# Optimization experiments

Hardware: AMD Instinct MI355X
Metric: run time of the kernel (lower is better)

The kernel has to match this reference:

```python
import jax, jax.numpy as jnp
import numpy as np

B, S, D = 4, 2048, 1024
H, HD = 16, 64
DFF = 4096
EPS = 1e-6


def setup_inputs() -> dict:
    key = jax.random.key(0)
    ks = jax.random.split(key, 16)
    sc = 0.02
    def w(k, shape):
        return jax.random.normal(k, shape, dtype=jnp.float32) * sc
    return {
        'x': jax.random.normal(ks[0], (B, S, D), dtype=jnp.float32),
        'wq': w(ks[1], (D, D)), 'bq': jnp.zeros((D,), jnp.float32),
        'wk': w(ks[2], (D, D)), 'bk': jnp.zeros((D,), jnp.float32),
        'wv': w(ks[3], (D, D)), 'bv': jnp.zeros((D,), jnp.float32),
        'wo': w(ks[4], (D, D)), 'bo': jnp.zeros((D,), jnp.float32),
        'w1': w(ks[5], (D, DFF)), 'b1': jnp.zeros((DFF,), jnp.float32),
        'w2': w(ks[6], (DFF, D)), 'b2': jnp.zeros((D,), jnp.float32),
        'ln1_a': jnp.ones((D,), jnp.float32), 'ln1_b': jnp.zeros((D,), jnp.float32),
        'ln2_a': jnp.ones((D,), jnp.float32), 'ln2_b': jnp.zeros((D,), jnp.float32),
    }


def layernorm(x, alpha, bias):
    # Matches torch module: std is unbiased (ddof=1), divide by (std + eps)
    mean = jnp.mean(x, axis=-1, keepdims=True)
    var = jnp.sum((x - mean) ** 2, axis=-1, keepdims=True) / (x.shape[-1] - 1)
    std = jnp.sqrt(var)
    return alpha * ((x - mean) / (std + EPS)) + bias


def mha(x, wq, bq, wk, bk, wv, bv, wo, bo):
    q = (x @ wq + bq).reshape(B, S, H, HD)
    k = (x @ wk + bk).reshape(B, S, H, HD)
    v = (x @ wv + bv).reshape(B, S, H, HD)
    scores = jnp.einsum('bqhd,bkhd->bhqk', q, k) / jnp.sqrt(jnp.float32(HD))
    attn = jax.nn.softmax(scores, axis=-1)
    out = jnp.einsum('bhqk,bkhd->bqhd', attn, v).reshape(B, S, D)
    return out @ wo + bo


def reference(x, wq, bq, wk, bk, wv, bv, wo, bo, w1, b1, w2, b2,
              ln1_a, ln1_b, ln2_a, ln2_b):
    # Residual 1: x + MHA(LN(x))   (dropout = identity, eval mode)
    x = x + mha(layernorm(x, ln1_a, ln1_b), wq, bq, wk, bk, wv, bv, wo, bo)
    # Residual 2: x + FFN(LN(x))
    h = layernorm(x, ln2_a, ln2_b)
    ffn = jax.nn.relu(h @ w1 + b1) @ w2 + b2
    return x + ffn
```

## Files before the change

### kernel.cpp

```cpp
#include <hip/hip_runtime.h>

#define S_ 2048
#define D_ 1024

typedef unsigned short u16;
typedef unsigned int u32;
typedef __bf16 bf16x8 __attribute__((ext_vector_type(8)));
typedef unsigned short us8 __attribute__((ext_vector_type(8)));
typedef unsigned short us4 __attribute__((ext_vector_type(4)));
typedef unsigned int u32x4 __attribute__((ext_vector_type(4)));
typedef float f32x4 __attribute__((ext_vector_type(4)));

#if __has_builtin(__builtin_amdgcn_exp2f)
#define EXP2(x) __builtin_amdgcn_exp2f(x)
#else
#define EXP2(x) exp2f(x)
#endif

static __device__ __forceinline__ u16 f2bf(float f) {
  unsigned u = __builtin_bit_cast(unsigned, f);
  u += 0x7fffu + ((u >> 16) & 1u);
  return (u16)(u >> 16);
}

static __device__ __forceinline__ unsigned cvtpk_bf16(float lo, float hi) {
  unsigned r;
  asm("v_cvt_pk_bf16_f32 %0, %1, %2" : "=v"(r) : "v"(lo), "v"(hi));
  return r;
}

static __device__ __forceinline__ f32x4 mfma16(bf16x8 a, bf16x8 b, f32x4 c) {
  return __builtin_amdgcn_mfma_f32_16x16x32_bf16(a, b, c, 0, 0, 0);
}

static __device__ __forceinline__ void gload16(const void* g, void* lds) {
  __builtin_amdgcn_global_load_lds((const __attribute__((address_space(1))) void*)g,
                                   (__attribute__((address_space(3))) void*)lds, 16, 0, 0);
}

__global__ __launch_bounds__(256) void prep_kernel(
    const float* __restrict__ wq, const float* __restrict__ wk, const float* __restrict__ wv,
    const float* __restrict__ wo, const float* __restrict__ w1, const float* __restrict__ w2,
    const float* __restrict__ bq, const float* __restrict__ bk, const float* __restrict__ bv,
    u16* __restrict__ wqkv, u16* __restrict__ wot, u16* __restrict__ w1t,
    u16* __restrict__ w2t, float* __restrict__ bcat, float qs) {
  const int bid = blockIdx.x;
  const int tx = threadIdx.x, ty = threadIdx.y;
  if (bid >= 12288) {
    const int i = (bid - 12288) * 256 + ty * 32 + tx;
    bcat[i] = (i < 1024) ? bq[i] * qs : ((i < 2048) ? bk[i - 1024] : bv[i - 2048]);
    return;
  }
  const float* in;
  u16* out;
  int K, N, idx;
  float sc = 1.0f;
  if (bid < 4096) {
    K = 1024; N = 1024; idx = bid & 1023;
    if (bid < 1024)      { in = wq; out = wqkv;             sc = qs; }
    else if (bid < 2048) { in = wk; out = wqkv + (1 << 20); }
    else if (bid < 3072) { in = wv; out = wqkv + (2 << 20); }
    else                 { in = wo; out = wot; }
  } else if (bid < 8192) {
    in = w1; out = w1t; K = 1024; N = 4096; idx = bid - 4096;
  } else {
    in = w2; out = w2t; K = 4096; N = 1024; idx = bid - 8192;
  }
  const int nb = N >> 5;
  const int n0 = (idx % nb) * 32, k0 = (idx / nb) * 32;
  __shared__ float t[32][33];
#pragma unroll
  for (int i = 0; i < 4; i++)
    t[ty + 8 * i][tx] = in[(size_t)(k0 + ty + 8 * i) * N + n0 + tx];
  __syncthreads();
#pragma unroll
  for (int i = 0; i < 4; i++)
    out[(size_t)(n0 + ty + 8 * i) * K + k0 + tx] = f2bf(t[tx][ty + 8 * i] * sc);
}

__global__ __launch_bounds__(256) void ln_kernel(const float* __restrict__ in,
                                                 u16* __restrict__ out,
                                                 const float* __restrict__ alpha,
                                                 const float* __restrict__ beta) {
  const int row = blockIdx.x;
  const int tid = threadIdx.x;
  const float4 v = *(const float4*)(in + (size_t)row * D_ + tid * 4);
  float s = v.x + v.y + v.z + v.w;
  float ss = v.x * v.x + v.y * v.y + v.z * v.z + v.w * v.w;
#pragma unroll
  for (int off = 32; off >= 1; off >>= 1) {
    s += __shfl_xor(s, off);
    ss += __shfl_xor(ss, off);
  }
  __shared__ float red[8];
  const int w = tid >> 6, lane = tid & 63;
  if (lane == 0) { red[w] = s; red[4 + w] = ss; }
  __syncthreads();
  s = red[0] + red[1] + red[2] + red[3];
  ss = red[4] + red[5] + red[6] + red[7];
  const float mean = s * (1.0f / D_);
  const float var = (ss - s * mean) * (1.0f / (D_ - 1));
  const float inv = 1.0f / (sqrtf(var) + 1e-6f);
  const int j = tid * 4;
  const float4 av = *(const float4*)(alpha + j);
  const float4 bv = *(const float4*)(beta + j);
  us4 o;
  o[0] = f2bf((v.x - mean) * inv * av.x + bv.x);
  o[1] = f2bf((v.y - mean) * inv * av.y + bv.y);
  o[2] = f2bf((v.z - mean) * inv * av.z + bv.z);
  o[3] = f2bf((v.w - mean) * inv * av.w + bv.w);
  *(us4*)(out + (size_t)row * D_ + j) = o;
}

template <int OM, bool RELU, bool RESID>
__global__ __launch_bounds__(512, 2) void gemm_bt(const u16* __restrict__ A,
                                                  const u16* __restrict__ Bt,
                                                  const float* __restrict__ bias,
                                                  const float* __restrict__ resid,
                                                  void* __restrict__ outp,
                                                  void* __restrict__ out1,
                                                  void* __restrict__ out2, int N, int K) {
  __shared__ u16 lds[3 * 24576];
  const int tid = threadIdx.x;
  const int lane = tid & 63, w = tid >> 6;
  const int g = lane >> 4, r = lane & 15;
  const int wr = w >> 1, wc = w & 1;

  const int gx = gridDim.x;
  const int nwg = gx * gridDim.y;
  const int orig = blockIdx.y * gx + blockIdx.x;
  const int nid = (orig & 7) * (nwg >> 3) + (orig >> 3);
  const int bx = nid % gx, by = nid / gx;
  const size_t row0 = (size_t)by * 256;
  const int col0 = bx * 128;

  float bias4[4];
#pragma unroll
  for (int n = 0; n < 4; n++) bias4[n] = bias[col0 + wc * 64 + n * 16 + r];

  f32x4 acc[4][4];
#pragma unroll
  for (int m = 0; m < 4; m++)
#pragma unroll
    for (int n = 0; n < 4; n++) {
      f32x4 z = {bias4[n], bias4[n], bias4[n], bias4[n]};
      acc[m][n] = z;
    }

  const int lrow = w * 8 + (lane >> 3);
  const int scol = 8 * ((lane & 7) ^ (lane >> 3));
  const u16* gA = A + (row0 + lrow) * (size_t)K + scol;
  const u16* gB = Bt + ((size_t)col0 + lrow) * (size_t)K + scol;
  const int nt = K >> 6;
  const int sw = (r & 7) << 3;

  int bufi = 0;
#pragma unroll
  for (int t0 = 0; t0 < 2; t0++) {
    u16* dA = lds + t0 * 24576 + w * 512;
#pragma unroll
    for (int j = 0; j < 4; j++) gload16(gA + (size_t)(j * 64) * K + t0 * 64, dA + j * 4096);
#pragma unroll
    for (int j = 0; j < 2; j++)
      gload16(gB + (size_t)(j * 64) * K + t0 * 64, dA + 16384 + j * 4096);
  }

  for (int t = 0; t < nt; ++t) {
    if (t + 1 < nt)
      asm volatile("s_waitcnt vmcnt(6)" ::: "memory");
    else
      asm volatile("s_waitcnt vmcnt(0)" ::: "memory");
    __builtin_amdgcn_s_barrier();
    asm volatile("" ::: "memory");
    const bool st = (t + 2 < nt);
    const int bn = (bufi + 2 >= 3) ? bufi - 1 : bufi + 2;
    u16* dS = lds + bn * 24576 + w * 512;
    const size_t ko = (size_t)(t + 2) * 64;
    const u16* As_ = lds + bufi * 24576;
    const u16* Bs_ = As_ + 16384;
    bf16x8 bfr[2][4];

#pragma unroll
    for (int p = 0; p < 4; ++p) {
      bf16x8 a0 = __builtin_bit_cast(
          bf16x8, *(const us8*)(As_ + (wr * 64 + p * 16 + r) * 64 + ((g * 8) ^ sw)));
      bf16x8 a1 = __builtin_bit_cast(
          bf16x8, *(const us8*)(As_ + (wr * 64 + p * 16 + r) * 64 + ((32 + g * 8) ^ sw)));
      if (p == 0) {
#pragma unroll
        for (int kk = 0; kk < 2; kk++)
#pragma unroll
          for (int n = 0; n < 4; n++)
            bfr[kk][n] = __builtin_bit_cast(
                bf16x8,
                *(const us8*)(Bs_ + (wc * 64 + n * 16 + r) * 64 + ((kk * 32 + g * 8) ^ sw)));
      }
      if (st) {
        if (p == 0) {
          gload16(gA + ko, dS);
          gload16(gA + (size_t)64 * K + ko, dS + 4096);
        } else if (p == 1) {
          gload16(gA + (size_t)128 * K + ko, dS + 8192);
          gload16(gA + (size_t)192 * K + ko, dS + 12288);
        } else if (p == 2) {
          gload16(gB + ko, dS + 16384);
          gload16(gB + (size_t)64 * K + ko, dS + 20480);
        }
      }
      asm volatile("s_waitcnt lgkmcnt(0)" ::: "memory");
      __builtin_amdgcn_sched_barrier(0);
      __builtin_amdgcn_s_setprio(1);
#pragma unroll
      for (int n = 0; n < 4; n++) {
        acc[p][n] = mfma16(a0, bfr[0][n], acc[p][n]);
        acc[p][n] = mfma16(a1, bfr[1][n], acc[p][n]);
      }
      __builtin_amdgcn_s_setprio(0);
      if (p < 3) __builtin_amdgcn_s_barrier();
    }
    bufi = (bufi == 2) ? 0 : bufi + 1;
  }

#pragma unroll
  for (int m = 0; m < 4; m++)
#pragma unroll
    for (int n = 0; n < 4; n++) {
      if (OM == 2) {
        const int seg = col0 >> 10;
        const int cl = (col0 & 1023) + wc * 64 + n * 16 + r;
        if (seg == 2) {
          const int head = cl >> 6, hd = cl & 63;
          const size_t rg0 = row0 + wr * 64 + m * 16 + 4 * g;
          const int b = (int)(rg0 >> 11), s0 = (int)(rg0 & 2047);
          us4 o;
#pragma unroll
          for (int i = 0; i < 4; i++) o[i] = f2bf(acc[m][n][i]);
          *(us4*)((u16*)out2 + (((size_t)(b * 16 + head) * 64 + hd) * S_ + s0)) = o;
        } else {
          u16* dst = (u16*)(seg == 0 ? outp : out1);
#pragma unroll
          for (int i = 0; i < 4; i++) {
            const size_t rg = row0 + wr * 64 + m * 16 + 4 * g + i;
            dst[rg * D_ + cl] = f2bf(acc[m][n][i]);
          }
        }
      } else {
#pragma unroll
        for (int i = 0; i < 4; i++) {
          const size_t rg = row0 + wr * 64 + m * 16 + 4 * g + i;
          const int cg = col0 + wc * 64 + n * 16 + r;
          float v = acc[m][n][i];
          if (RESID) v += resid[rg * N + cg];
          if (RELU) v = fmaxf(v, 0.0f);
          if (OM == 1)
            ((float*)outp)[rg * N + cg] = v;
          else
            ((u16*)outp)[rg * N + cg] = f2bf(v);
        }
      }
    }
}

template <bool RELU>
__global__ __launch_bounds__(512, 2) void gemm_bt256(const u16* __restrict__ A,
                                                     const u16* __restrict__ Bt,
                                                     const float* __restrict__ bias,
                                                     u16* __restrict__ outp, int N, int K) {
  __shared__ u16 lds[2 * 32768];
  const int tid = threadIdx.x;
  const int lane = tid & 63, w = tid >> 6;
  const int g = lane >> 4, r = lane & 15;
  const int wr = w >> 2, wc = w & 3;
  const int gx = gridDim.x;
  const int nwg = gx * gridDim.y;
  const int orig = blockIdx.y * gx + blockIdx.x;
  const int nid = (orig & 7) * (nwg >> 3) + (orig >> 3);
  const int bx = nid % gx, by = nid / gx;
  const size_t row0 = (size_t)by * 256;
  const int col0 = bx * 256;

  float bias4[4];
#pragma unroll
  for (int n = 0; n < 4; n++) bias4[n] = bias[col0 + wc * 64 + n * 16 + r];

  f32x4 acc[8][4];
#pragma unroll
  for (int m = 0; m < 8; m++)
#pragma unroll
    for (int n = 0; n < 4; n++) {
      f32x4 z = {bias4[n], bias4[n], bias4[n], bias4[n]};
      acc[m][n] = z;
    }

  const int lrow = tid >> 3;
  const int scol = 8 * ((tid & 7) ^ (lrow & 7));
  const u16* gA = A + (row0 + lrow) * (size_t)K + scol;
  const u16* gB = Bt + ((size_t)col0 + lrow) * (size_t)K + scol;
  const int nt = K >> 6;
  const int sw = (r & 7) << 3;

  {
    u16* d = lds + w * 512;
#pragma unroll
    for (int j = 0; j < 4; j++) gload16(gA + (size_t)(j * 64) * K, d + j * 4096);
#pragma unroll
    for (int j = 0; j < 4; j++) gload16(gB + (size_t)(j * 64) * K, d + 16384 + j * 4096);
  }

  for (int t = 0; t < nt; ++t) {
    const u16* As_ = lds + (t & 1) * 32768;
    const u16* Bs_ = As_ + 16384;
    if (t + 1 < nt) {
      u16* d = lds + ((t + 1) & 1) * 32768 + w * 512;
      const size_t ko = (size_t)(t + 1) * 64;
#pragma unroll
      for (int j = 0; j < 4; j++) gload16(gA + (size_t)(j * 64) * K + ko, d + j * 4096);
#pragma unroll
      for (int j = 0; j < 4; j++) gload16(gB + (size_t)(j * 64) * K + ko, d + 16384 + j * 4096);
      asm volatile("s_waitcnt vmcnt(8)" ::: "memory");
    } else {
      asm volatile("s_waitcnt vmcnt(0)" ::: "memory");
    }
    __builtin_amdgcn_s_barrier();
    asm volatile("" ::: "memory");

    bf16x8 bfr[2][4];
#pragma unroll
    for (int kk = 0; kk < 2; kk++)
#pragma unroll
      for (int n = 0; n < 4; n++)
        bfr[kk][n] = __builtin_bit_cast(
            bf16x8, *(const us8*)(Bs_ + (wc * 64 + n * 16 + r) * 64 + ((kk * 32 + g * 8) ^ sw)));

#pragma unroll
    for (int p = 0; p < 4; ++p) {
      bf16x8 af[2][2];
#pragma unroll
      for (int mm = 0; mm < 2; mm++) {
        const int row = wr * 128 + (p * 2 + mm) * 16 + r;
        af[0][mm] = __builtin_bit_cast(bf16x8, *(const us8*)(As_ + row * 64 + ((g * 8) ^ sw)));
        af[1][mm] =
            __builtin_bit_cast(bf16x8, *(const us8*)(As_ + row * 64 + ((32 + g * 8) ^ sw)));
      }
      asm volatile("" ::: "memory");
      if (p > 0) __builtin_amdgcn_s_barrier();
      asm volatile("s_waitcnt lgkmcnt(0)" ::: "memory");
      __builtin_amdgcn_sched_barrier(0);
      __builtin_amdgcn_s_setprio(1);
#pragma unroll
      for (int mm = 0; mm < 2; mm++)
#pragma unroll
        for (int n = 0; n < 4; n++) {
          acc[p * 2 + mm][n] = mfma16(af[0][mm], bfr[0][n], acc[p * 2 + mm][n]);
          acc[p * 2 + mm][n] = mfma16(af[1][mm], bfr[1][n], acc[p * 2 + mm][n]);
        }
      __builtin_amdgcn_s_setprio(0);
    }
    asm volatile("" ::: "memory");
    __builtin_amdgcn_s_barrier();
  }

#pragma unroll
  for (int m = 0; m < 8; m++)
#pragma unroll
    for (int n = 0; n < 4; n++)
#pragma unroll
      for (int i = 0; i < 4; i++) {
        const size_t rg = row0 + wr * 128 + m * 16 + 4 * g + i;
        const int cg = col0 + wc * 64 + n * 16 + r;
        float v = acc[m][n][i];
        if (RELU) v = fmaxf(v, 0.0f);
        outp[rg * N + cg] = f2bf(v);
      }
}

__global__ __launch_bounds__(256) void attn_kernel(const u16* __restrict__ Q,
                                                   const u16* __restrict__ Km,
                                                   const u16* __restrict__ Vt_g,
                                                   u16* __restrict__ O) {
  __shared__ u16 Klds[2 * 4096];
  __shared__ u16 Vlds[2 * 4352];
  const int tid = threadIdx.x;
  const int lane = tid & 63, w = tid >> 6;
  const int g = lane >> 4, r = lane & 15;
  const int bh = blockIdx.y;
  const int b = bh >> 4, head = bh & 15;
  const size_t rowbase = (size_t)b * S_;
  const int colbase = head * 64;
  const int qw = blockIdx.x * 128 + w * 32;

  bf16x8 qf0[2], qf1[2];
#pragma unroll
  for (int qh = 0; qh < 2; qh++) {
    const u16* qrow = Q + (rowbase + qw + qh * 16 + r) * D_ + colbase;
    qf0[qh] = __builtin_bit_cast(bf16x8, *(const us8*)(qrow + g * 8));
    qf1[qh] = __builtin_bit_cast(bf16x8, *(const us8*)(qrow + 32 + g * 8));
  }

  const int srow = tid >> 3;
  const int sslot = (tid & 7) ^ (srow & 7);
  const u16* Kg = Km + (rowbase + srow) * D_ + colbase + sslot * 8;
  const u16* Vg = Vt_g + ((size_t)bh * 64 + srow) * S_ + (tid & 7) * 8;

  const us8 onesw = {0x3F80, 0x3F80, 0x3F80, 0x3F80, 0x3F80, 0x3F80, 0x3F80, 0x3F80};
  const bf16x8 ones8 = __builtin_bit_cast(bf16x8, onesw);

  f32x4 lacc[2];
  f32x4 oacc[2][4];
#pragma unroll
  for (int qh = 0; qh < 2; qh++) {
    f32x4 z = {0.0f, 0.0f, 0.0f, 0.0f};
    lacc[qh] = z;
#pragma unroll
    for (int n = 0; n < 4; n++) oacc[qh][n] = z;
  }

  {
    const us8 pv0 = *(const us8*)(Vg);
    const us8 pv1 = *(const us8*)(Vg + 32 * S_);
    gload16(Kg, (char*)Klds + w * 1024);
    gload16(Kg + (size_t)32 * D_, (char*)Klds + w * 1024 + 4096);
    *(us8*)(Vlds + srow * 68 + (tid & 7) * 8) = pv0;
    *(us8*)(Vlds + (srow + 32) * 68 + (tid & 7) * 8) = pv1;
    __syncthreads();
  }

  for (int kt = 0; kt < S_ / 64; kt++) {
    const int cur = kt & 1, nxt = cur ^ 1;
    const bool more = (kt + 1 < S_ / 64);
    us8 nv0, nv1;
    if (more) {
      nv0 = *(const us8*)(Vg + (size_t)(kt + 1) * 64);
      nv1 = *(const us8*)(Vg + 32 * S_ + (size_t)(kt + 1) * 64);
      gload16(Kg + (size_t)(kt + 1) * 64 * D_, (char*)Klds + nxt * 8192 + w * 1024);
      gload16(Kg + (size_t)((kt + 1) * 64 + 32) * D_,
              (char*)Klds + nxt * 8192 + w * 1024 + 4096);
    }
    const u16* Kc = Klds + cur * 4096;
    const u16* Vc = Vlds + cur * 4352;

    f32x4 st[4][2];
    __builtin_amdgcn_s_setprio(1);
#pragma unroll
    for (int f = 0; f < 4; f++) {
      const int row = f * 16 + r;
      const int sw = row & 7;
      const bf16x8 k0 = __builtin_bit_cast(bf16x8, *(const us8*)(Kc + row * 64 + (g ^ sw) * 8));
      const bf16x8 k1 =
          __builtin_bit_cast(bf16x8, *(const us8*)(Kc + row * 64 + ((g + 4) ^ sw) * 8));
#pragma unroll
      for (int qh = 0; qh < 2; qh++) {
        f32x4 z = {0.0f, 0.0f, 0.0f, 0.0f};
        st[f][qh] = mfma16(k0, qf0[qh], z);
        st[f][qh] = mfma16(k1, qf1[qh], st[f][qh]);
      }
    }
    __builtin_amdgcn_s_setprio(0);
    u32 pw[2][8];
#pragma unroll
    for (int qh = 0; qh < 2; qh++)
#pragma unroll
      for (int f = 0; f < 4; f++) {
        const float e0 = EXP2(st[f][qh][0]);
        const float e1 = EXP2(st[f][qh][1]);
        const float e2 = EXP2(st[f][qh][2]);
        const float e3 = EXP2(st[f][qh][3]);
        pw[qh][f * 2] = cvtpk_bf16(e0, e1);
        pw[qh][f * 2 + 1] = cvtpk_bf16(e2, e3);
      }
    if (more) {
      *(us8*)(Vlds + nxt * 4352 + srow * 68 + (tid & 7) * 8) = nv0;
      *(us8*)(Vlds + nxt * 4352 + (srow + 32) * 68 + (tid & 7) * 8) = nv1;
    }

    bf16x8 a0[2], a1[2];
#pragma unroll
    for (int qh = 0; qh < 2; qh++) {
      const u32x4 a0w = {pw[qh][0], pw[qh][1], pw[qh][2], pw[qh][3]};
      const u32x4 a1w = {pw[qh][4], pw[qh][5], pw[qh][6], pw[qh][7]};
      a0[qh] = __builtin_bit_cast(bf16x8, a0w);
      a1[qh] = __builtin_bit_cast(bf16x8, a1w);
    }
    __builtin_amdgcn_s_setprio(1);
#pragma unroll
    for (int qh = 0; qh < 2; qh++) {
      lacc[qh] = mfma16(a0[qh], ones8, lacc[qh]);
      lacc[qh] = mfma16(a1[qh], ones8, lacc[qh]);
    }
#pragma unroll
    for (int n = 0; n < 4; n++) {
      const u16* vr = Vc + (n * 16 + r) * 68;
      const us4 v00 = *(const us4*)(vr + g * 4);
      const us4 v01 = *(const us4*)(vr + 16 + g * 4);
      const us4 v10 = *(const us4*)(vr + 32 + g * 4);
      const us4 v11 = *(const us4*)(vr + 48 + g * 4);
      const bf16x8 vb0 =
          __builtin_bit_cast(bf16x8, __builtin_shufflevector(v00, v01, 0, 1, 2, 3, 4, 5, 6, 7));
      const bf16x8 vb1 =
          __builtin_bit_cast(bf16x8, __builtin_shufflevector(v10, v11, 0, 1, 2, 3, 4, 5, 6, 7));
#pragma unroll
      for (int qh = 0; qh < 2; qh++) {
        oacc[qh][n] = mfma16(a0[qh], vb0, oacc[qh][n]);
        oacc[qh][n] = mfma16(a1[qh], vb1, oacc[qh][n]);
      }
    }
    __builtin_amdgcn_s_setprio(0);
    asm volatile("s_waitcnt vmcnt(0) lgkmcnt(0)" ::: "memory");
    __builtin_amdgcn_s_barrier();
    asm volatile("" ::: "memory");
  }

#pragma unroll
  for (int qh = 0; qh < 2; qh++) {
    float ld[4];
#pragma unroll
    for (int i = 0; i < 4; i++) ld[i] = 1.0f / lacc[qh][i];
#pragma unroll
    for (int n = 0; n < 4; n++)
#pragma unroll
      for (int i = 0; i < 4; i++)
        O[(rowbase + qw + qh * 16 + 4 * g + i) * D_ + colbase + n * 16 + r] =
            f2bf(oacc[qh][n][i] * ld[i]);
  }
}

extern "C" void kernel_launch(void* const* d_in, const int* in_sizes, int n_in, void* d_out,
                              int out_size, void* d_ws, size_t ws_size, hipStream_t stream) {
  (void)in_sizes; (void)n_in; (void)out_size; (void)ws_size;
  const float* x = (const float*)d_in[0];
  const float* wq = (const float*)d_in[1];
  const float* bq = (const float*)d_in[2];
  const float* wk = (const float*)d_in[3];
  const float* bk = (const float*)d_in[4];
  const float* wv = (const float*)d_in[5];
  const float* bv = (const float*)d_in[6];
  const float* wo = (const float*)d_in[7];
  const float* bo = (const float*)d_in[8];
  const float* w1 = (const float*)d_in[9];
  const float* b1 = (const float*)d_in[10];
  const float* w2 = (const float*)d_in[11];
  const float* b2 = (const float*)d_in[12];
  const float* ln1a = (const float*)d_in[13];
  const float* ln1b = (const float*)d_in[14];
  const float* ln2a = (const float*)d_in[15];
  const float* ln2b = (const float*)d_in[16];

  char* ws = (char*)d_ws;
  const size_t MB = 1ull << 20;
  u16* wqkv = (u16*)(ws + 0 * MB);
  u16* wot = (u16*)(ws + 6 * MB);
  u16* w1t = (u16*)(ws + 8 * MB);
  u16* w2t = (u16*)(ws + 16 * MB);
  u16* xA = (u16*)(ws + 24 * MB);
  u16* qb = (u16*)(ws + 40 * MB);
  u16* kb = (u16*)(ws + 56 * MB);
  u16* vt = (u16*)(ws + 72 * MB);
  float* bcat = (float*)(ws + 88 * MB);
  u16* ff1 = (u16*)(ws + 40 * MB);
  float* x1 = (float*)(ws + 104 * MB);

  const float QSCALE = 0.125f * 1.4426950408889634f;

  prep_kernel<<<12300, dim3(32, 8), 0, stream>>>(wq, wk, wv, wo, w1, w2, bq, bk, bv, wqkv, wot,
                                                 w1t, w2t, bcat, QSCALE);

  ln_kernel<<<8192, 256, 0, stream>>>(x, xA, ln1a, ln1b);
  gemm_bt<2, false, false><<<dim3(24, 32), 512, 0, stream>>>(xA, wqkv, bcat, nullptr, qb, kb, vt,
                                                             3072, 1024);
  attn_kernel<<<dim3(16, 64), 256, 0, stream>>>(qb, kb, vt, xA);
  gemm_bt<1, false, true><<<dim3(8, 32), 512, 0, stream>>>(xA, wot, bo, x, x1, nullptr, nullptr,
                                                           1024, 1024);
  ln_kernel<<<8192, 256, 0, stream>>>(x1, xA, ln2a, ln2b);
  gemm_bt256<true><<<dim3(16, 32), 512, 0, stream>>>(xA, w1t, b1, ff1, 4096, 1024);
  gemm_bt<1, false, true><<<dim3(8, 32), 512, 0, stream>>>(ff1, w2t, b2, x1, (float*)d_out,
                                                           nullptr, nullptr, 1024, 4096);
}
```

Before: 370.5 us.

## Software-pipeline attention: defer PV by one tile, async V loads, permuted V^T layout

The QKV GEMM epilogue now writes V^T with a permuted sequence index, so each 8-element chunk is directly the bf16x8 operand the PV MFMA expects. The attention kernel then loads V with direct-to-LDS gload16 into a swizzled, unpadded buffer instead of register round-trips and shuffles. The loop is restructured so the PV and row-sum MFMAs for tile kt-1 run after the QK^T of tile kt, and K is prefetched two tiles ahead using partial vmcnt waits. The aim is to hide exp and load latency behind MFMA work, at the cost of an extra barrier per iteration and more complex wait accounting.

```diff
diff --git a/kernel.cpp b/kernel.cpp
--- a/kernel.cpp
+++ b/kernel.cpp
@@ -232,10 +232,11 @@
           const int head = cl >> 6, hd = cl & 63;
           const size_t rg0 = row0 + wr * 64 + m * 16 + 4 * g;
           const int b = (int)(rg0 >> 11), s0 = (int)(rg0 & 2047);
+          const int s0p = (s0 & ~63) | (s0 & 32) | ((s0 << 1) & 24) | ((s0 >> 2) & 4);
           us4 o;
 #pragma unroll
           for (int i = 0; i < 4; i++) o[i] = f2bf(acc[m][n][i]);
-          *(us4*)((u16*)out2 + (((size_t)(b * 16 + head) * 64 + hd) * S_ + s0)) = o;
+          *(us4*)((u16*)out2 + (((size_t)(b * 16 + head) * 64 + hd) * S_ + s0p)) = o;
         } else {
           u16* dst = (u16*)(seg == 0 ? outp : out1);
 #pragma unroll
@@ -379,7 +380,7 @@
                                                    const u16* __restrict__ Vt_g,
                                                    u16* __restrict__ O) {
   __shared__ u16 Klds[2 * 4096];
-  __shared__ u16 Vlds[2 * 4352];
+  __shared__ u16 Vlds[2 * 4096];
   const int tid = threadIdx.x;
   const int lane = tid & 63, w = tid >> 6;
   const int g = lane >> 4, r = lane & 15;
@@ -400,7 +401,9 @@
   const int srow = tid >> 3;
   const int sslot = (tid & 7) ^ (srow & 7);
   const u16* Kg = Km + (rowbase + srow) * D_ + colbase + sslot * 8;
-  const u16* Vg = Vt_g + ((size_t)bh * 64 + srow) * S_ + (tid & 7) * 8;
+  const u16* Vg = Vt_g + ((size_t)bh * 64 + srow) * S_ + sslot * 8;
+  char* lK = (char*)Klds + w * 1024;
+  char* lV = (char*)Vlds + w * 1024;
 
   const us8 onesw = {0x3F80, 0x3F80, 0x3F80, 0x3F80, 0x3F80, 0x3F80, 0x3F80, 0x3F80};
   const bf16x8 ones8 = __builtin_bit_cast(bf16x8, onesw);
@@ -415,39 +418,32 @@
     for (int n = 0; n < 4; n++) oacc[qh][n] = z;
   }
 
-  {
-    const us8 pv0 = *(const us8*)(Vg);
-    const us8 pv1 = *(const us8*)(Vg + 32 * S_);
-    gload16(Kg, (char*)Klds + w * 1024);
-    gload16(Kg + (size_t)32 * D_, (char*)Klds + w * 1024 + 4096);
-    *(us8*)(Vlds + srow * 68 + (tid & 7) * 8) = pv0;
-    *(us8*)(Vlds + (srow + 32) * 68 + (tid & 7) * 8) = pv1;
-    __syncthreads();
-  }
-
-  for (int kt = 0; kt < S_ / 64; kt++) {
-    const int cur = kt & 1, nxt = cur ^ 1;
-    const bool more = (kt + 1 < S_ / 64);
-    us8 nv0, nv1;
-    if (more) {
-      nv0 = *(const us8*)(Vg + (size_t)(kt + 1) * 64);
-      nv1 = *(const us8*)(Vg + 32 * S_ + (size_t)(kt + 1) * 64);
-      gload16(Kg + (size_t)(kt + 1) * 64 * D_, (char*)Klds + nxt * 8192 + w * 1024);
-      gload16(Kg + (size_t)((kt + 1) * 64 + 32) * D_,
-              (char*)Klds + nxt * 8192 + w * 1024 + 4096);
-    }
-    const u16* Kc = Klds + cur * 4096;
-    const u16* Vc = Vlds + cur * 4352;
+  constexpr int NT = S_ / 64;
+  gload16(Kg, lK);
+  gload16(Kg + (size_t)32 * D_, lK + 4096);
+  gload16(Vg, lV);
+  gload16(Vg + (size_t)32 * S_, lV + 4096);
+  gload16(Kg + (size_t)64 * D_, lK + 8192);
+  gload16(Kg + (size_t)96 * D_, lK + 8192 + 4096);
+  asm volatile("s_waitcnt vmcnt(2)" ::: "memory");
+  __builtin_amdgcn_s_barrier();
+  asm volatile("" ::: "memory");
+
+  bf16x8 pa0[2], pa1[2];
+
+  for (int kt = 0; kt < NT; ++kt) {
+    const u16* Kc = Klds + (kt & 1) * 4096;
+    const u16* Vp = Vlds + ((kt - 1) & 1) * 4096;
 
     f32x4 st[4][2];
     __builtin_amdgcn_s_setprio(1);
 #pragma unroll
     for (int f = 0; f < 4; f++) {
       const int row = f * 16 + r;
-      const int sw = row & 7;
-      const bf16x8 k0 = __builtin_bit_cast(bf16x8, *(const us8*)(Kc + row * 64 + (g ^ sw) * 8));
+      const int sw7 = row & 7;
+      const bf16x8 k0 = __builtin_bit_cast(bf16x8, *(const us8*)(Kc + row * 64 + (g ^ sw7) * 8));
       const bf16x8 k1 =
-          __builtin_bit_cast(bf16x8, *(const us8*)(Kc + row * 64 + ((g + 4) ^ sw) * 8));
+          __builtin_bit_cast(bf16x8, *(const us8*)(Kc + row * 64 + ((g + 4) ^ sw7) * 8));
 #pragma unroll
       for (int qh = 0; qh < 2; qh++) {
         f32x4 z = {0.0f, 0.0f, 0.0f, 0.0f};
@@ -456,6 +452,31 @@
       }
     }
     __builtin_amdgcn_s_setprio(0);
+
+    if (kt > 0) {
+      __builtin_amdgcn_s_setprio(1);
+#pragma unroll
+      for (int qh = 0; qh < 2; qh++) {
+        lacc[qh] = mfma16(pa0[qh], ones8, lacc[qh]);
+        lacc[qh] = mfma16(pa1[qh], ones8, lacc[qh]);
+      }
+#pragma unroll
+      for (int n = 0; n < 4; n++) {
+        const int row = n * 16 + r;
+        const int sw7 = r & 7;
+        const bf16x8 vb0 =
+            __builtin_bit_cast(bf16x8, *(const us8*)(Vp + row * 64 + (g ^ sw7) * 8));
+        const bf16x8 vb1 =
+            __builtin_bit_cast(bf16x8, *(const us8*)(Vp + row * 64 + ((4 + g) ^ sw7) * 8));
+#pragma unroll
+        for (int qh = 0; qh < 2; qh++) {
+          oacc[qh][n] = mfma16(pa0[qh], vb0, oacc[qh][n]);
+          oacc[qh][n] = mfma16(pa1[qh], vb1, oacc[qh][n]);
+        }
+      }
+      __builtin_amdgcn_s_setprio(0);
+    }
+
     u32 pw[2][8];
 #pragma unroll
     for (int qh = 0; qh < 2; qh++)
@@ -468,46 +489,57 @@
         pw[qh][f * 2] = cvtpk_bf16(e0, e1);
         pw[qh][f * 2 + 1] = cvtpk_bf16(e2, e3);
       }
-    if (more) {
-      *(us8*)(Vlds + nxt * 4352 + srow * 68 + (tid & 7) * 8) = nv0;
-      *(us8*)(Vlds + nxt * 4352 + (srow + 32) * 68 + (tid & 7) * 8) = nv1;
-    }
-
-    bf16x8 a0[2], a1[2];
 #pragma unroll
     for (int qh = 0; qh < 2; qh++) {
       const u32x4 a0w = {pw[qh][0], pw[qh][1], pw[qh][2], pw[qh][3]};
       const u32x4 a1w = {pw[qh][4], pw[qh][5], pw[qh][6], pw[qh][7]};
-      a0[qh] = __builtin_bit_cast(bf16x8, a0w);
-      a1[qh] = __builtin_bit_cast(bf16x8, a1w);
-    }
-    __builtin_amdgcn_s_setprio(1);
-#pragma unroll
-    for (int qh = 0; qh < 2; qh++) {
-      lacc[qh] = mfma16(a0[qh], ones8, lacc[qh]);
-      lacc[qh] = mfma16(a1[qh], ones8, lacc[qh]);
-    }
-#pragma unroll
-    for (int n = 0; n < 4; n++) {
-      const u16* vr = Vc + (n * 16 + r) * 68;
-      const us4 v00 = *(const us4*)(vr + g * 4);
-      const us4 v01 = *(const us4*)(vr + 16 + g * 4);
-      const us4 v10 = *(const us4*)(vr + 32 + g * 4);
-      const us4 v11 = *(const us4*)(vr + 48 + g * 4);
-      const bf16x8 vb0 =
-          __builtin_bit_cast(bf16x8, __builtin_shufflevector(v00, v01, 0, 1, 2, 3, 4, 5, 6, 7));
-      const bf16x8 vb1 =
-          __builtin_bit_cast(bf16x8, __builtin_shufflevector(v10, v11, 0, 1, 2, 3, 4, 5, 6, 7));
-#pragma unroll
-      for (int qh = 0; qh < 2; qh++) {
-        oacc[qh][n] = mfma16(a0[qh], vb0, oacc[qh][n]);
-        oacc[qh][n] = mfma16(a1[qh], vb1, oacc[qh][n]);
-      }
-    }
-    __builtin_amdgcn_s_setprio(0);
-    asm volatile("s_waitcnt vmcnt(0) lgkmcnt(0)" ::: "memory");
+      pa0[qh] = __builtin_bit_cast(bf16x8, a0w);
+      pa1[qh] = __builtin_bit_cast(bf16x8, a1w);
+    }
+
     __builtin_amdgcn_s_barrier();
     asm volatile("" ::: "memory");
+
+    if (kt + 2 < NT) {
+      gload16(Kg + (size_t)(kt + 2) * 64 * D_, (char*)Klds + (kt & 1) * 8192 + w * 1024);
+      gload16(Kg + (size_t)((kt + 2) * 64 + 32) * D_,
+              (char*)Klds + (kt & 1) * 8192 + w * 1024 + 4096);
+    }
+    if (kt + 1 < NT) {
+      gload16(Vg + (size_t)(kt + 1) * 64, (char*)Vlds + ((kt + 1) & 1) * 8192 + w * 1024);
+      gload16(Vg + (size_t)32 * S_ + (size_t)(kt + 1) * 64,
+              (char*)Vlds + ((kt + 1) & 1) * 8192 + w * 1024 + 4096);
+    }
+    if (kt + 2 < NT)
+      asm volatile("s_waitcnt vmcnt(4)" ::: "memory");
+    else if (kt + 1 < NT)
+      asm volatile("s_waitcnt vmcnt(2)" ::: "memory");
+    else
+      asm volatile("s_waitcnt vmcnt(0)" ::: "memory");
+    __builtin_amdgcn_s_barrier();
+    asm volatile("" ::: "memory");
+  }
+
+  {
+    const u16* Vp = Vlds + ((NT - 1) & 1) * 4096;
+#pragma unroll
+    for (int qh = 0; qh < 2; qh++) {
+      lacc[qh] = mfma16(pa0[qh], ones8, lacc[qh]);
+      lacc[qh] = mfma16(pa1[qh], ones8, lacc[qh]);
+    }
+#pragma unroll
+    for (int n = 0; n < 4; n++) {
+      const int row = n * 16 + r;
+      const int sw7 = r & 7;
+      const bf16x8 vb0 = __builtin_bit_cast(bf16x8, *(const us8*)(Vp + row * 64 + (g ^ sw7) * 8));
+      const bf16x8 vb1 =
+          __builtin_bit_cast(bf16x8, *(const us8*)(Vp + row * 64 + ((4 + g) ^ sw7) * 8));
+#pragma unroll
+      for (int qh = 0; qh < 2; qh++) {
+        oacc[qh][n] = mfma16(pa0[qh], vb0, oacc[qh][n]);
+        oacc[qh][n] = mfma16(pa1[qh], vb1, oacc[qh][n]);
+      }
+    }
   }
 
 #pragma unroll
```

Result: no change. 366.3 us (-1.1%).
